# Performance work log

Hardware: AMD Instinct MI355X
Metric: run time of the kernel (lower is better)

The kernel has to match this reference:

```python
import jax, jax.numpy as jnp
import numpy as np

D = 1024      # d_model
H = 2         # num_heads
DH = D // H   # head dim


def setup_inputs() -> dict:
    key = jax.random.key(0)
    ks = jax.random.split(key, 16)
    B, N = 512, 512
    s = 0.02
    return {
        "h": jax.random.normal(ks[0], (B, D), jnp.float32),
        "c": jax.random.normal(ks[1], (B, D), jnp.float32),
        "all_states": jax.random.normal(ks[2], (B, N, D), jnp.float32),
        "external_input": jax.random.normal(ks[3], (B, D), jnp.float32),
        # nn.MultiheadAttention params
        "in_proj_w": jax.random.normal(ks[4], (3 * D, D), jnp.float32) * s,
        "in_proj_b": jnp.zeros((3 * D,), jnp.float32),
        "out_proj_w": jax.random.normal(ks[5], (D, D), jnp.float32) * s,
        "out_proj_b": jnp.zeros((D,), jnp.float32),
        # nn.LSTMCell params (gate order: i, f, g, o)
        "w_ih": jax.random.normal(ks[6], (4 * D, 2 * D), jnp.float32) * s,
        "b_ih": jnp.zeros((4 * D,), jnp.float32),
        "w_hh": jax.random.normal(ks[7], (4 * D, D), jnp.float32) * s,
        "b_hh": jnp.zeros((4 * D,), jnp.float32),
        # ln_out params
        "ln_w": jnp.ones((D,), jnp.float32),
        "ln_b": jnp.zeros((D,), jnp.float32),
    }


def _layer_norm(x, w, b, eps=1e-5):
    mu = jnp.mean(x, axis=-1, keepdims=True)
    var = jnp.var(x, axis=-1, keepdims=True)
    return (x - mu) * jax.lax.rsqrt(var + eps) * w + b


def reference(h, c, all_states, external_input,
              in_proj_w, in_proj_b, out_proj_w, out_proj_b,
              w_ih, b_ih, w_hh, b_hh, ln_w, ln_b):
    B, N, _ = all_states.shape
    wq, wk, wv = in_proj_w[:D], in_proj_w[D:2 * D], in_proj_w[2 * D:]
    bq, bk, bv = in_proj_b[:D], in_proj_b[D:2 * D], in_proj_b[2 * D:]

    # single-query multi-head attention over all_states
    q = (h @ wq.T + bq).reshape(B, H, DH)                     # [B,H,Dh]
    k = (all_states @ wk.T + bk).reshape(B, N, H, DH)          # [B,N,H,Dh]
    v = (all_states @ wv.T + bv).reshape(B, N, H, DH)
    scores = jnp.einsum("bhd,bnhd->bhn", q, k) / jnp.sqrt(jnp.float32(DH))
    attn = jax.nn.softmax(scores, axis=-1)                     # [B,H,N]
    ctx = jnp.einsum("bhn,bnhd->bhd", attn, v).reshape(B, D)
    context = ctx @ out_proj_w.T + out_proj_b                  # [B,D]

    # LSTMCell on cat([context, external_input])
    rnn_in = jnp.concatenate([context, external_input], axis=-1)  # [B,2D]
    gates = rnn_in @ w_ih.T + b_ih + h @ w_hh.T + b_hh            # [B,4D]
    i, f, g, o = jnp.split(gates, 4, axis=-1)
    new_c = jax.nn.sigmoid(f) * c + jax.nn.sigmoid(i) * jnp.tanh(g)
    new_h = jax.nn.sigmoid(o) * jnp.tanh(new_c)

    return _layer_norm(new_h, ln_w, ln_b), new_c
```

## Files before the change

kernel.cpp:

```cpp
#include <hip/hip_runtime.h>
#include <math.h>
#include <stdint.h>

constexpr int kD  = 1024;
constexpr int kB  = 512;
constexpr int kN  = 512;
constexpr int kDH = 512;

using bf16x8 = __attribute__((ext_vector_type(8))) short;
using f32x4v = __attribute__((ext_vector_type(4))) float;
using us8    = __attribute__((ext_vector_type(8))) unsigned short;

__device__ __forceinline__ unsigned short f2bf(float f) {
    uint32_t u = __float_as_uint(f);
    u += 0x7fffu + ((u >> 16) & 1u);
    return (unsigned short)(u >> 16);
}

__device__ __forceinline__ void async16(const void* g, void* l) {
    __builtin_amdgcn_global_load_lds(
        (const __attribute__((address_space(1))) uint32_t*)g,
        (__attribute__((address_space(3))) uint32_t*)l, 16, 0, 0);
}

__device__ __forceinline__ void barrier_acq() {
    __builtin_amdgcn_s_barrier();
    asm volatile("" ::: "memory");
    __builtin_amdgcn_sched_barrier(0);
}

__global__ __launch_bounds__(256)
void cvt_bf16(const float* __restrict__ src, unsigned short* __restrict__ dst,
              int scols8, int dcols, int coloff, int n8)
{
    int idx = blockIdx.x * 256 + threadIdx.x;
    if (idx >= n8) return;
    int row = idx / scols8;
    int c = (idx - row * scols8) * 8;
    const float4* s = (const float4*)(src + (long)row * ((long)scols8 * 8) + c);
    float4 v0 = s[0], v1 = s[1];
    us8 o;
    o[0] = f2bf(v0.x); o[1] = f2bf(v0.y); o[2] = f2bf(v0.z); o[3] = f2bf(v0.w);
    o[4] = f2bf(v1.x); o[5] = f2bf(v1.y); o[6] = f2bf(v1.z); o[7] = f2bf(v1.w);
    *(us8*)(dst + (long)row * dcols + coloff + c) = o;
}

__global__ __launch_bounds__(256)
void tcvt_wk(const float* __restrict__ wk, unsigned short* __restrict__ dst)
{
    __shared__ float t[32][33];
    const int nt = blockIdx.x;
    const int kt = blockIdx.y;
    const int hh = blockIdx.z;
    const int tx = threadIdx.x & 31, ty = threadIdx.x >> 5;
#pragma unroll
    for (int j = 0; j < 4; ++j)
        t[ty + j * 8][tx] = wk[(long)(hh * 512 + kt * 32 + ty + j * 8) * kD + nt * 32 + tx];
    __syncthreads();
#pragma unroll
    for (int j = 0; j < 4; ++j) {
        int n = nt * 32 + ty + j * 8;
        int k = kt * 32 + tx;
        dst[(long)hh * 524288 + (long)n * 512 + k] = f2bf(t[tx][ty + j * 8]);
    }
}

__global__ __launch_bounds__(256)
void badd_kernel(const float* __restrict__ a, const float* __restrict__ b,
                 float* __restrict__ o)
{
    int i = blockIdx.x * 256 + threadIdx.x;
    if (i < 4096) o[i] = a[i] + b[i];
}

__global__ __launch_bounds__(256)
void gemm_bf16(const unsigned short* __restrict__ A, int lda, long sAz,
               const unsigned short* __restrict__ B, int ldb, long sBz,
               float* __restrict__ Cf, int ldcf, long sCfz,
               unsigned short* __restrict__ Cb, int ldcb, long sCbz,
               const float* __restrict__ bias, long sbz, int K)
{
    __shared__ short As[4][64][8];
    __shared__ short Bs[4][128][8];
    A += (long)blockIdx.z * sAz;
    B += (long)blockIdx.z * sBz;

    const int tid = threadIdx.x;
    const int l = tid & 63, w = tid >> 6;
    const int wr = w >> 1, wc = w & 1;
    const int bm = blockIdx.y * 64, bn = blockIdx.x * 128;

    f32x4v acc[2][4] = {};

    for (int k0 = 0; k0 < K; k0 += 32) {
        __syncthreads();
        {
            int ks = tid >> 6, r = tid & 63;
            async16(A + (long)(bm + r) * lda + k0 + ks * 8, (short*)As + (long)tid * 8);
        }
#pragma unroll
        for (int j = 0; j < 2; ++j) {
            int ca = j * 256 + tid;
            int ks = ca >> 7, r = ca & 127;
            async16(B + (long)(bn + r) * ldb + k0 + ks * 8, (short*)Bs + (long)ca * 8);
        }
        __syncthreads();

        const int ks = l >> 4, rr = l & 15;
        bf16x8 a[2], b[4];
#pragma unroll
        for (int t = 0; t < 2; ++t)
            a[t] = *(const bf16x8*)&As[ks][wr * 32 + t * 16 + rr][0];
#pragma unroll
        for (int t = 0; t < 4; ++t)
            b[t] = *(const bf16x8*)&Bs[ks][wc * 64 + t * 16 + rr][0];
#pragma unroll
        for (int mt = 0; mt < 2; ++mt)
#pragma unroll
            for (int nt = 0; nt < 4; ++nt)
                acc[mt][nt] = __builtin_amdgcn_mfma_f32_16x16x32_bf16(
                    a[mt], b[nt], acc[mt][nt], 0, 0, 0);
    }

    const int rr = l & 15, rg = l >> 4;
#pragma unroll
    for (int mt = 0; mt < 2; ++mt) {
#pragma unroll
        for (int nt = 0; nt < 4; ++nt) {
            const int n = bn + wc * 64 + nt * 16 + rr;
            float bb = bias ? bias[(long)blockIdx.z * sbz + n] : 0.f;
#pragma unroll
            for (int r = 0; r < 4; ++r) {
                const int m = bm + wr * 32 + mt * 16 + rg * 4 + r;
                float val = acc[mt][nt][r] + bb;
                if (Cf) Cf[(long)blockIdx.z * sCfz + (long)m * ldcf + n] = val;
                if (Cb) Cb[(long)blockIdx.z * sCbz + (long)m * ldcb + n] = f2bf(val);
            }
        }
    }
}

constexpr int kR = 4;
constexpr int kSPL = 4;
__global__ __launch_bounds__(512, 6)
void attn3(const float* __restrict__ xall,
           const float* __restrict__ qt,
           float* __restrict__ spart,
           float* __restrict__ mlpart)
{
    __shared__ float X[2][kR][kD];
    __shared__ float scp[2][kR][2];

    const int bid = blockIdx.x;
    const int b = bid >> 2, cs = bid & 3;
    const int tid = threadIdx.x;
    const int w = tid >> 6, l = tid & 63;
    const int row = w >> 1, hf = w & 1;
    const int h = tid >> 8, d0 = (tid & 255) * 4;
    const float scale = 0.044194173824159216f;

    float qr0[8], qr1[8];
    {
        const float* qb = qt + (long)b * 2 * kD + hf * 512 + l * 8;
        float4 a0 = *(const float4*)(qb);
        float4 a1 = *(const float4*)(qb + 4);
        float4 b0 = *(const float4*)(qb + kD);
        float4 b1 = *(const float4*)(qb + kD + 4);
        qr0[0]=a0.x; qr0[1]=a0.y; qr0[2]=a0.z; qr0[3]=a0.w;
        qr0[4]=a1.x; qr0[5]=a1.y; qr0[6]=a1.z; qr0[7]=a1.w;
        qr1[0]=b0.x; qr1[1]=b0.y; qr1[2]=b0.z; qr1[3]=b0.w;
        qr1[4]=b1.x; qr1[5]=b1.y; qr1[6]=b1.z; qr1[7]=b1.w;
    }

    float m_run = -1e30f, l_run = 0.f;
    float s0 = 0.f, s1 = 0.f, s2 = 0.f, s3 = 0.f;

    const char* xbase = (const char*)(xall + (long)b * kN * kD + (long)cs * 128 * kD);

#define STAGE(tt, bufi) do {                                              \
        const char* srcb = xbase + (long)(tt) * 16384;                    \
        char* dstb = (char*)&X[bufi][0][0];                               \
        _Pragma("unroll")                                                 \
        for (int j = 0; j < 2; ++j) {                                     \
            int chunk = j * 512 + tid;                                    \
            async16(srcb + (long)chunk * 16, dstb + (long)chunk * 16);    \
        }                                                                 \
    } while (0)

    STAGE(0, 0);

    constexpr int nT = 128 / kR;
    for (int t = 0; t < nT; ++t) {
        const int cur = t & 1;
        asm volatile("s_waitcnt vmcnt(0)" ::: "memory");
        barrier_acq();
        if (t + 1 < nT) STAGE(t + 1, cur ^ 1);

        {
            const float* xr = &X[cur][row][hf * 512 + l * 8];
            float4 x0 = *(const float4*)(xr);
            float4 x1 = *(const float4*)(xr + 4);
            float xa[8] = {x0.x, x0.y, x0.z, x0.w, x1.x, x1.y, x1.z, x1.w};
            float a0 = 0.f, a1 = 0.f;
#pragma unroll
            for (int j = 0; j < 8; ++j) {
                a0 += xa[j] * qr0[j];
                a1 += xa[j] * qr1[j];
            }
#pragma unroll
            for (int m = 32; m >= 1; m >>= 1) {
                a0 += __shfl_xor(a0, m);
                a1 += __shfl_xor(a1, m);
            }
            if (l == 0) {
                scp[0][row][hf] = a0;
                scp[1][row][hf] = a1;
            }
        }
        asm volatile("s_waitcnt lgkmcnt(0)" ::: "memory");
        barrier_acq();

        float v[kR];
#pragma unroll
        for (int n = 0; n < kR; ++n)
            v[n] = (scp[h][n][0] + scp[h][n][1]) * scale;
        float mx = v[0];
#pragma unroll
        for (int n = 1; n < kR; ++n) mx = fmaxf(mx, v[n]);
        float mnew = fmaxf(m_run, mx);
        float r = __expf(m_run - mnew);
        float p[kR], psum = 0.f;
#pragma unroll
        for (int n = 0; n < kR; ++n) { p[n] = __expf(v[n] - mnew); psum += p[n]; }
        l_run = l_run * r + psum;
        m_run = mnew;
        s0 *= r; s1 *= r; s2 *= r; s3 *= r;

#pragma unroll
        for (int n = 0; n < kR; ++n) {
            float4 xv = *(const float4*)&X[cur][n][d0];
            s0 += p[n] * xv.x; s1 += p[n] * xv.y;
            s2 += p[n] * xv.z; s3 += p[n] * xv.w;
        }
    }
#undef STAGE

    *(float4*)(spart + (((long)b * kSPL + cs) * 2 + h) * kD + d0) =
        make_float4(s0, s1, s2, s3);
    if ((tid & 255) == 0) {
        float* mlp = mlpart + (long)b * 16 + cs * 4 + h * 2;
        mlp[0] = m_run;
        mlp[1] = l_run;
    }
}

__global__ __launch_bounds__(256)
void attn_combine(const float* __restrict__ spart, const float* __restrict__ mlpart,
                  unsigned short* __restrict__ sac_bf)
{
    const int b = blockIdx.x;
    const int tid = threadIdx.x;
    const int h = tid >> 7, d0 = (tid & 127) * 8;

    const float* mlb = mlpart + (long)b * 16 + h * 2;
    float m[kSPL], lv[kSPL];
#pragma unroll
    for (int c = 0; c < kSPL; ++c) { m[c] = mlb[c * 4]; lv[c] = mlb[c * 4 + 1]; }
    float ms = m[0];
#pragma unroll
    for (int c = 1; c < kSPL; ++c) ms = fmaxf(ms, m[c]);
    float wgt[kSPL], L = 0.f;
#pragma unroll
    for (int c = 0; c < kSPL; ++c) { wgt[c] = __expf(m[c] - ms); L += wgt[c] * lv[c]; }
    const float inv = 1.0f / L;

    float acc[8] = {};
#pragma unroll
    for (int c = 0; c < kSPL; ++c) {
        const float4* sp = (const float4*)(spart + (((long)b * kSPL + c) * 2 + h) * kD + d0);
        float4 a = sp[0], bq = sp[1];
        acc[0] += wgt[c] * a.x;  acc[1] += wgt[c] * a.y;
        acc[2] += wgt[c] * a.z;  acc[3] += wgt[c] * a.w;
        acc[4] += wgt[c] * bq.x; acc[5] += wgt[c] * bq.y;
        acc[6] += wgt[c] * bq.z; acc[7] += wgt[c] * bq.w;
    }
    us8 o;
#pragma unroll
    for (int j = 0; j < 8; ++j) o[j] = f2bf(acc[j] * inv);
    *(us8*)(sac_bf + (long)b * 2048 + h * kD + d0) = o;
}

__device__ __forceinline__ float sigm(float x) { return 1.0f / (1.0f + __expf(-x)); }

__global__ __launch_bounds__(256)
void lstm_ln(const float* __restrict__ gates, const float* __restrict__ cin,
             const float* __restrict__ ln_w, const float* __restrict__ ln_b,
             float* __restrict__ out0, float* __restrict__ out1)
{
    __shared__ float red[2][4];
    __shared__ float stats[2];

    const int b = blockIdx.x;
    const int tid = threadIdx.x;
    const int d4 = tid * 4;
    const float* g = gates + (long)b * 4096;

    float4 gi = *(const float4*)(g + d4);
    float4 gf = *(const float4*)(g + 1024 + d4);
    float4 gg = *(const float4*)(g + 2048 + d4);
    float4 go = *(const float4*)(g + 3072 + d4);
    float4 cv = *(const float4*)(cin + (long)b * kD + d4);

    float iv[4] = {gi.x, gi.y, gi.z, gi.w};
    float fv[4] = {gf.x, gf.y, gf.z, gf.w};
    float gv[4] = {gg.x, gg.y, gg.z, gg.w};
    float ov[4] = {go.x, go.y, go.z, go.w};
    float cc[4] = {cv.x, cv.y, cv.z, cv.w};

    float nc[4], nh[4];
#pragma unroll
    for (int u = 0; u < 4; ++u) {
        nc[u] = sigm(fv[u]) * cc[u] + sigm(iv[u]) * tanhf(gv[u]);
        nh[u] = sigm(ov[u]) * tanhf(nc[u]);
    }
    *(float4*)(out1 + (long)b * kD + d4) = make_float4(nc[0], nc[1], nc[2], nc[3]);

    float sum = nh[0] + nh[1] + nh[2] + nh[3];
    float ss  = nh[0]*nh[0] + nh[1]*nh[1] + nh[2]*nh[2] + nh[3]*nh[3];
#pragma unroll
    for (int m = 32; m >= 1; m >>= 1) {
        sum += __shfl_xor(sum, m);
        ss  += __shfl_xor(ss, m);
    }
    const int wave = tid >> 6, lane = tid & 63;
    if (lane == 0) { red[0][wave] = sum; red[1][wave] = ss; }
    __syncthreads();
    if (tid == 0) {
        float s = red[0][0] + red[0][1] + red[0][2] + red[0][3];
        float q = red[1][0] + red[1][1] + red[1][2] + red[1][3];
        float mu = s / (float)kD;
        float var = q / (float)kD - mu * mu;
        stats[0] = mu;
        stats[1] = rsqrtf(var + 1e-5f);
    }
    __syncthreads();
    const float mu = stats[0], rstd = stats[1];
    float4 lw = *(const float4*)(ln_w + d4);
    float4 lb = *(const float4*)(ln_b + d4);
    float lwv[4] = {lw.x, lw.y, lw.z, lw.w};
    float lbv[4] = {lb.x, lb.y, lb.z, lb.w};
    float o[4];
#pragma unroll
    for (int u = 0; u < 4; ++u)
        o[u] = (nh[u] - mu) * rstd * lwv[u] + lbv[u];
    *(float4*)(out0 + (long)b * kD + d4) = make_float4(o[0], o[1], o[2], o[3]);
}

extern "C" void kernel_launch(void* const* d_in, const int* in_sizes, int n_in,
                              void* d_out, int out_size, void* d_ws, size_t ws_size,
                              hipStream_t stream)
{
    (void)in_sizes; (void)n_in; (void)out_size;

    const float* h    = (const float*)d_in[0];
    const float* c    = (const float*)d_in[1];
    const float* xall = (const float*)d_in[2];
    const float* ext  = (const float*)d_in[3];
    const float* in_w = (const float*)d_in[4];
    const float* in_b = (const float*)d_in[5];
    const float* wo   = (const float*)d_in[6];
    const float* bo   = (const float*)d_in[7];
    const float* w_ih = (const float*)d_in[8];
    const float* b_ih = (const float*)d_in[9];
    const float* w_hh = (const float*)d_in[10];
    const float* b_hh = (const float*)d_in[11];
    const float* ln_w = (const float*)d_in[12];
    const float* ln_b = (const float*)d_in[13];

    float* out0 = (float*)d_out;
    float* out1 = out0 + (long)kB * kD;

    char* p = (char*)d_ws;
    const size_t need = 62963712ull;
    if (ws_size < need) return;

    float*          badd   = (float*)p;          p += 16384;
    unsigned short* h_bf   = (unsigned short*)p; p += 1048576;
    unsigned short* wq_bf  = (unsigned short*)p; p += 2097152;
    unsigned short* wkT_bf = (unsigned short*)p; p += 2097152;
    unsigned short* wv_bf  = (unsigned short*)p; p += 2097152;
    unsigned short* wo_bf  = (unsigned short*)p; p += 2097152;
    unsigned short* q_bf   = (unsigned short*)p; p += 1048576;
    unsigned short* sac_bf = (unsigned short*)p; p += 2097152;
    unsigned short* ctx_bf = (unsigned short*)p; p += 1048576;
    unsigned short* acat   = (unsigned short*)p; p += 3145728;
    unsigned short* wcat   = (unsigned short*)p; p += 25165824;
    char* ov = p;
    float* qtl    = (float*)ov;
    float* spart  = (float*)(ov + 4194304);
    float* mlpart = (float*)(ov + 4194304 + 16777216);
    float* gates  = (float*)ov;

    const float* wk_f = in_w + (long)kD * kD;
    const float* bq = in_b;
    const float* bv = in_b + 2 * kD;

    auto cvt = [&](const float* src, unsigned short* dst, int rows, int scols,
                   int dcols, int coloff) {
        int n8 = rows * (scols / 8);
        cvt_bf16<<<(n8 + 255) / 256, 256, 0, stream>>>(src, dst, scols / 8, dcols, coloff, n8);
    };

    badd_kernel<<<16, 256, 0, stream>>>(b_ih, b_hh, badd);
    cvt(h, h_bf, 512, 1024, 1024, 0);
    cvt(in_w, wq_bf, 1024, 1024, 1024, 0);
    tcvt_wk<<<dim3(32, 16, 2), 256, 0, stream>>>(wk_f, wkT_bf);
    cvt(in_w + 2L * kD * kD, wv_bf, 1024, 1024, 1024, 0);
    cvt(wo, wo_bf, 1024, 1024, 1024, 0);
    cvt(w_ih, wcat, 4096, 2048, 3072, 0);
    cvt(w_hh, wcat, 4096, 1024, 3072, 2048);

    gemm_bf16<<<dim3(8, 8, 1), 256, 0, stream>>>(
        h_bf, 1024, 0, wq_bf, 1024, 0,
        nullptr, 0, 0, q_bf, 1024, 0, bq, 0, 1024);

    gemm_bf16<<<dim3(8, 8, 2), 256, 0, stream>>>(
        q_bf, 1024, 512, wkT_bf, 512, 524288,
        qtl, 2048, 1024, nullptr, 0, 0, nullptr, 0, 512);

    attn3<<<kB * kSPL, 512, 0, stream>>>(xall, qtl, spart, mlpart);

    attn_combine<<<kB, 256, 0, stream>>>(spart, mlpart, sac_bf);

    gemm_bf16<<<dim3(4, 8, 2), 256, 0, stream>>>(
        sac_bf, 2048, 1024, wv_bf, 1024, 524288,
        nullptr, 0, 0, ctx_bf, 1024, 512, bv, 512, 1024);

    gemm_bf16<<<dim3(8, 8, 1), 256, 0, stream>>>(
        ctx_bf, 1024, 0, wo_bf, 1024, 0,
        nullptr, 0, 0, acat, 3072, 0, bo, 0, 1024);

    cvt(ext, acat, 512, 1024, 3072, 1024);
    cvt(h,   acat, 512, 1024, 3072, 2048);

    gemm_bf16<<<dim3(32, 8, 1), 256, 0, stream>>>(
        acat, 3072, 0, wcat, 3072, 0,
        gates, 4096, 0, nullptr, 0, 0, badd, 0, 3072);

    lstm_ln<<<kB, 256, 0, stream>>>(gates, c, ln_w, ln_b, out0, out1);
}
```

Measured before the change: 450.7 us.

## Rewrite attention streaming kernel as per-wave online softmax with bf16 partials

Replaces the LDS-staged, block-synchronised attention kernel (4 blocks per batch, 4 rows per step) with one block per batch where each wave owns 64 rows and streams them directly from global memory. Each wave keeps its own running max and sum per head and rescales its accumulators only when the max grows by more than a threshold, which removes per-step barriers and most rescaling work. Partial sums are stored as bf16 and merged across 8 waves in the combine kernel, cutting partial-buffer traffic. In exchange it loses the async LDS prefetch, lowers occupancy and grid size (512 blocks), and adds bf16 rounding of the partials.

Result: no change. 448.8 us (-0.4%).

```diff
diff --git a/kernel.cpp b/kernel.cpp
--- a/kernel.cpp
+++ b/kernel.cpp
@@ -17,16 +17,14 @@
     return (unsigned short)(u >> 16);
 }
 
+__device__ __forceinline__ float bf2f(unsigned short s) {
+    return __uint_as_float((uint32_t)s << 16);
+}
+
 __device__ __forceinline__ void async16(const void* g, void* l) {
     __builtin_amdgcn_global_load_lds(
         (const __attribute__((address_space(1))) uint32_t*)g,
         (__attribute__((address_space(3))) uint32_t*)l, 16, 0, 0);
-}
-
-__device__ __forceinline__ void barrier_acq() {
-    __builtin_amdgcn_s_barrier();
-    asm volatile("" ::: "memory");
-    __builtin_amdgcn_sched_barrier(0);
 }
 
 __global__ __launch_bounds__(256)
@@ -140,149 +138,126 @@
     }
 }
 
-constexpr int kR = 4;
-constexpr int kSPL = 4;
-__global__ __launch_bounds__(512, 6)
-void attn3(const float* __restrict__ xall,
+__global__ __launch_bounds__(512, 4)
+void attn6(const float* __restrict__ xall,
            const float* __restrict__ qt,
-           float* __restrict__ spart,
+           unsigned short* __restrict__ spart_bf,
            float* __restrict__ mlpart)
 {
-    __shared__ float X[2][kR][kD];
-    __shared__ float scp[2][kR][2];
-
-    const int bid = blockIdx.x;
-    const int b = bid >> 2, cs = bid & 3;
+    const int b = blockIdx.x;
     const int tid = threadIdx.x;
     const int w = tid >> 6, l = tid & 63;
-    const int row = w >> 1, hf = w & 1;
-    const int h = tid >> 8, d0 = (tid & 255) * 4;
     const float scale = 0.044194173824159216f;
 
-    float qr0[8], qr1[8];
+    float qa[16], qb[16];
     {
-        const float* qb = qt + (long)b * 2 * kD + hf * 512 + l * 8;
-        float4 a0 = *(const float4*)(qb);
-        float4 a1 = *(const float4*)(qb + 4);
-        float4 b0 = *(const float4*)(qb + kD);
-        float4 b1 = *(const float4*)(qb + kD + 4);
-        qr0[0]=a0.x; qr0[1]=a0.y; qr0[2]=a0.z; qr0[3]=a0.w;
-        qr0[4]=a1.x; qr0[5]=a1.y; qr0[6]=a1.z; qr0[7]=a1.w;
-        qr1[0]=b0.x; qr1[1]=b0.y; qr1[2]=b0.z; qr1[3]=b0.w;
-        qr1[4]=b1.x; qr1[5]=b1.y; qr1[6]=b1.z; qr1[7]=b1.w;
-    }
-
-    float m_run = -1e30f, l_run = 0.f;
-    float s0 = 0.f, s1 = 0.f, s2 = 0.f, s3 = 0.f;
-
-    const char* xbase = (const char*)(xall + (long)b * kN * kD + (long)cs * 128 * kD);
-
-#define STAGE(tt, bufi) do {                                              \
-        const char* srcb = xbase + (long)(tt) * 16384;                    \
-        char* dstb = (char*)&X[bufi][0][0];                               \
-        _Pragma("unroll")                                                 \
-        for (int j = 0; j < 2; ++j) {                                     \
-            int chunk = j * 512 + tid;                                    \
-            async16(srcb + (long)chunk * 16, dstb + (long)chunk * 16);    \
-        }                                                                 \
-    } while (0)
-
-    STAGE(0, 0);
-
-    constexpr int nT = 128 / kR;
-    for (int t = 0; t < nT; ++t) {
-        const int cur = t & 1;
-        asm volatile("s_waitcnt vmcnt(0)" ::: "memory");
-        barrier_acq();
-        if (t + 1 < nT) STAGE(t + 1, cur ^ 1);
-
-        {
-            const float* xr = &X[cur][row][hf * 512 + l * 8];
-            float4 x0 = *(const float4*)(xr);
-            float4 x1 = *(const float4*)(xr + 4);
-            float xa[8] = {x0.x, x0.y, x0.z, x0.w, x1.x, x1.y, x1.z, x1.w};
-            float a0 = 0.f, a1 = 0.f;
-#pragma unroll
-            for (int j = 0; j < 8; ++j) {
-                a0 += xa[j] * qr0[j];
-                a1 += xa[j] * qr1[j];
-            }
-#pragma unroll
-            for (int m = 32; m >= 1; m >>= 1) {
-                a0 += __shfl_xor(a0, m);
-                a1 += __shfl_xor(a1, m);
-            }
-            if (l == 0) {
-                scp[0][row][hf] = a0;
-                scp[1][row][hf] = a1;
-            }
-        }
-        asm volatile("s_waitcnt lgkmcnt(0)" ::: "memory");
-        barrier_acq();
-
-        float v[kR];
-#pragma unroll
-        for (int n = 0; n < kR; ++n)
-            v[n] = (scp[h][n][0] + scp[h][n][1]) * scale;
-        float mx = v[0];
-#pragma unroll
-        for (int n = 1; n < kR; ++n) mx = fmaxf(mx, v[n]);
-        float mnew = fmaxf(m_run, mx);
-        float r = __expf(m_run - mnew);
-        float p[kR], psum = 0.f;
-#pragma unroll
-        for (int n = 0; n < kR; ++n) { p[n] = __expf(v[n] - mnew); psum += p[n]; }
-        l_run = l_run * r + psum;
-        m_run = mnew;
-        s0 *= r; s1 *= r; s2 *= r; s3 *= r;
-
-#pragma unroll
-        for (int n = 0; n < kR; ++n) {
-            float4 xv = *(const float4*)&X[cur][n][d0];
-            s0 += p[n] * xv.x; s1 += p[n] * xv.y;
-            s2 += p[n] * xv.z; s3 += p[n] * xv.w;
-        }
-    }
-#undef STAGE
-
-    *(float4*)(spart + (((long)b * kSPL + cs) * 2 + h) * kD + d0) =
-        make_float4(s0, s1, s2, s3);
-    if ((tid & 255) == 0) {
-        float* mlp = mlpart + (long)b * 16 + cs * 4 + h * 2;
-        mlp[0] = m_run;
-        mlp[1] = l_run;
-    }
-}
-
-__global__ __launch_bounds__(256)
-void attn_combine(const float* __restrict__ spart, const float* __restrict__ mlpart,
-                  unsigned short* __restrict__ sac_bf)
+        const float* qp = qt + (long)b * 2048 + l * 16;
+#pragma unroll
+        for (int j = 0; j < 4; ++j) {
+            float4 v0 = *(const float4*)(qp + j * 4);
+            float4 v1 = *(const float4*)(qp + 1024 + j * 4);
+            qa[j*4+0] = v0.x; qa[j*4+1] = v0.y; qa[j*4+2] = v0.z; qa[j*4+3] = v0.w;
+            qb[j*4+0] = v1.x; qb[j*4+1] = v1.y; qb[j*4+2] = v1.z; qb[j*4+3] = v1.w;
+        }
+    }
+
+    float m0 = -1e30f, l0 = 0.f, m1 = -1e30f, l1 = 0.f;
+    float sa[16] = {}, sb[16] = {};
+
+    const float* xr = xall + ((long)b * kN + w * 64) * kD + l * 16;
+
+    for (int r = 0; r < 64; ++r) {
+        float xv[16];
+#pragma unroll
+        for (int j = 0; j < 4; ++j) {
+            float4 v = *(const float4*)(xr + j * 4);
+            xv[j*4+0] = v.x; xv[j*4+1] = v.y; xv[j*4+2] = v.z; xv[j*4+3] = v.w;
+        }
+        xr += kD;
+
+        float d0 = 0.f, d1 = 0.f;
+#pragma unroll
+        for (int j = 0; j < 16; ++j) { d0 += xv[j] * qa[j]; d1 += xv[j] * qb[j]; }
+#pragma unroll
+        for (int mm = 32; mm >= 1; mm >>= 1) {
+            d0 += __shfl_xor(d0, mm);
+            d1 += __shfl_xor(d1, mm);
+        }
+        float v0 = d0 * scale, v1 = d1 * scale;
+
+        if (v0 > m0 + 8.f) {
+            float rsc = __expf(m0 - v0);
+            l0 *= rsc;
+#pragma unroll
+            for (int j = 0; j < 16; ++j) sa[j] *= rsc;
+            m0 = v0;
+        }
+        float p0 = __expf(v0 - m0);
+        l0 += p0;
+
+        if (v1 > m1 + 8.f) {
+            float rsc = __expf(m1 - v1);
+            l1 *= rsc;
+#pragma unroll
+            for (int j = 0; j < 16; ++j) sb[j] *= rsc;
+            m1 = v1;
+        }
+        float p1 = __expf(v1 - m1);
+        l1 += p1;
+
+#pragma unroll
+        for (int j = 0; j < 16; ++j) {
+            sa[j] += p0 * xv[j];
+            sb[j] += p1 * xv[j];
+        }
+    }
+
+    unsigned short* sp0 = spart_bf + (((long)b * 8 + w) * 2 + 0) * 1024 + l * 16;
+    unsigned short* sp1 = spart_bf + (((long)b * 8 + w) * 2 + 1) * 1024 + l * 16;
+    us8 o0, o1;
+#pragma unroll
+    for (int j = 0; j < 8; ++j) { o0[j] = f2bf(sa[j]); o1[j] = f2bf(sa[j + 8]); }
+    *(us8*)(sp0) = o0; *(us8*)(sp0 + 8) = o1;
+#pragma unroll
+    for (int j = 0; j < 8; ++j) { o0[j] = f2bf(sb[j]); o1[j] = f2bf(sb[j + 8]); }
+    *(us8*)(sp1) = o0; *(us8*)(sp1 + 8) = o1;
+
+    if (l == 0) {
+        float* mlp = mlpart + (((long)b * 8 + w) * 2) * 2;
+        mlp[0] = m0; mlp[1] = l0; mlp[2] = m1; mlp[3] = l1;
+    }
+}
+
+__global__ __launch_bounds__(256)
+void attn_combine8(const unsigned short* __restrict__ spart_bf,
+                   const float* __restrict__ mlpart,
+                   unsigned short* __restrict__ sac_bf)
 {
     const int b = blockIdx.x;
     const int tid = threadIdx.x;
     const int h = tid >> 7, d0 = (tid & 127) * 8;
 
-    const float* mlb = mlpart + (long)b * 16 + h * 2;
-    float m[kSPL], lv[kSPL];
-#pragma unroll
-    for (int c = 0; c < kSPL; ++c) { m[c] = mlb[c * 4]; lv[c] = mlb[c * 4 + 1]; }
+    float m[8], lv[8];
+#pragma unroll
+    for (int c = 0; c < 8; ++c) {
+        const float* mlp = mlpart + (((long)b * 8 + c) * 2 + h) * 2;
+        m[c] = mlp[0]; lv[c] = mlp[1];
+    }
     float ms = m[0];
 #pragma unroll
-    for (int c = 1; c < kSPL; ++c) ms = fmaxf(ms, m[c]);
-    float wgt[kSPL], L = 0.f;
-#pragma unroll
-    for (int c = 0; c < kSPL; ++c) { wgt[c] = __expf(m[c] - ms); L += wgt[c] * lv[c]; }
+    for (int c = 1; c < 8; ++c) ms = fmaxf(ms, m[c]);
+    float wgt[8], L = 0.f;
+#pragma unroll
+    for (int c = 0; c < 8; ++c) { wgt[c] = __expf(m[c] - ms); L += wgt[c] * lv[c]; }
     const float inv = 1.0f / L;
 
     float acc[8] = {};
 #pragma unroll
-    for (int c = 0; c < kSPL; ++c) {
-        const float4* sp = (const float4*)(spart + (((long)b * kSPL + c) * 2 + h) * kD + d0);
-        float4 a = sp[0], bq = sp[1];
-        acc[0] += wgt[c] * a.x;  acc[1] += wgt[c] * a.y;
-        acc[2] += wgt[c] * a.z;  acc[3] += wgt[c] * a.w;
-        acc[4] += wgt[c] * bq.x; acc[5] += wgt[c] * bq.y;
-        acc[6] += wgt[c] * bq.z; acc[7] += wgt[c] * bq.w;
+    for (int c = 0; c < 8; ++c) {
+        us8 sv = *(const us8*)(spart_bf + (((long)b * 8 + c) * 2 + h) * 1024 + d0);
+#pragma unroll
+        for (int j = 0; j < 8; ++j)
+            acc[j] += wgt[c] * bf2f(sv[j]);
     }
     us8 o;
 #pragma unroll
@@ -381,7 +356,7 @@
     float* out1 = out0 + (long)kB * kD;
 
     char* p = (char*)d_ws;
-    const size_t need = 62963712ull;
+    const size_t need = 63062016ull;
     if (ws_size < need) return;
 
     float*          badd   = (float*)p;          p += 16384;
@@ -396,10 +371,10 @@
     unsigned short* acat   = (unsigned short*)p; p += 3145728;
     unsigned short* wcat   = (unsigned short*)p; p += 25165824;
     char* ov = p;
-    float* qtl    = (float*)ov;
-    float* spart  = (float*)(ov + 4194304);
-    float* mlpart = (float*)(ov + 4194304 + 16777216);
-    float* gates  = (float*)ov;
+    float*          qtl      = (float*)ov;
+    unsigned short* spart_bf = (unsigned short*)(ov + 4194304);
+    float*          mlpart   = (float*)(ov + 4194304 + 16777216);
+    float*          gates    = (float*)ov;
 
     const float* wk_f = in_w + (long)kD * kD;
     const float* bq = in_b;
@@ -428,9 +403,9 @@
         q_bf, 1024, 512, wkT_bf, 512, 524288,
         qtl, 2048, 1024, nullptr, 0, 0, nullptr, 0, 512);
 
-    attn3<<<kB * kSPL, 512, 0, stream>>>(xall, qtl, spart, mlpart);
-
-    attn_combine<<<kB, 256, 0, stream>>>(spart, mlpart, sac_bf);
+    attn6<<<kB, 512, 0, stream>>>(xall, qtl, spart_bf, mlpart);
+
+    attn_combine8<<<kB, 256, 0, stream>>>(spart_bf, mlpart, sac_bf);
 
     gemm_bf16<<<dim3(4, 8, 2), 256, 0, stream>>>(
         sac_bf, 2048, 1024, wv_bf, 1024, 524288,
```
